# Kernel tuning notes

Hardware: AMD Instinct MI355X
Metric: run time of the kernel (lower is better)

Reference implementation:

```python
import jax, jax.numpy as jnp
import numpy as np

DIM = 512
HEADS = 8
DIM_HEAD = 64
ROT_DIM = DIM_HEAD // 2  # RotaryEmbedding(dim_head // 2)
B = 4
N = 8192


def rotate_every_two(x):
    # '... (d j) -> ... d j', j=2 ; (x1, x2) -> (-x2, x1) interleaved back
    x1 = x[..., 0::2]
    x2 = x[..., 1::2]
    return jnp.stack((-x2, x1), axis=-1).reshape(x.shape)


def apply_rotary_emb(freqs, t):
    # freqs: [1,1,n,rot_dim]; rotary on first rot_dim channels, passthrough rest
    rot_dim = freqs.shape[-1]
    t_rot, t_pass = t[..., :rot_dim], t[..., rot_dim:]
    t_rot = t_rot * jnp.cos(freqs) + rotate_every_two(t_rot) * jnp.sin(freqs)
    return jnp.concatenate((t_rot, t_pass), axis=-1)


def rotary_freqs(n):
    # lucidrains RotaryEmbedding(ROT_DIM): inv_freq over ROT_DIM//2, repeated r=2
    inv_freq = 1.0 / (10000.0 ** (jnp.arange(0, ROT_DIM, 2, dtype=jnp.float32) / ROT_DIM))
    f = jnp.arange(n, dtype=jnp.float32)[:, None] * inv_freq[None, :]  # [n, ROT_DIM//2]
    return jnp.repeat(f, 2, axis=-1)  # [n, ROT_DIM]


def setup_inputs() -> dict:
    key = jax.random.key(0)
    ks = jax.random.split(key, 8)
    inner = HEADS * DIM_HEAD
    s = lambda fan_in: 1.0 / np.sqrt(fan_in)
    return {
        "x": jax.random.normal(ks[0], (B, N, DIM), dtype=jnp.float32),
        "w_qkv": jax.random.uniform(ks[1], (DIM, inner * 3), jnp.float32, -s(DIM), s(DIM)),
        "w_q_logits": jax.random.uniform(ks[2], (DIM_HEAD, 1), jnp.float32, -s(DIM_HEAD), s(DIM_HEAD)),
        "w_k_logits": jax.random.uniform(ks[3], (DIM_HEAD // 2, 1), jnp.float32, -s(DIM_HEAD // 2), s(DIM_HEAD // 2)),
        "w_r": jax.random.uniform(ks[4], (DIM_HEAD // 2, DIM_HEAD), jnp.float32, -s(DIM_HEAD // 2), s(DIM_HEAD // 2)),
        "b_r": jax.random.uniform(ks[5], (DIM_HEAD,), jnp.float32, -s(DIM_HEAD // 2), s(DIM_HEAD // 2)),
        "w_out": jax.random.uniform(ks[6], (inner, DIM), jnp.float32, -s(inner), s(inner)),
        "b_out": jax.random.uniform(ks[7], (DIM,), jnp.float32, -s(inner), s(inner)),
    }


def reference(x, w_qkv, w_q_logits, w_k_logits, w_r, b_r, w_out, b_out):
    b, n, _ = x.shape
    h, d = HEADS, DIM_HEAD
    scale = d ** -0.5

    qkv = x @ w_qkv  # [b,n,3*h*d]
    q, k, v = jnp.split(qkv, 3, axis=-1)
    to_bhnd = lambda t: t.reshape(b, n, h, d).transpose(0, 2, 1, 3)
    q, k, v = to_bhnd(q), to_bhnd(k), to_bhnd(v)

    freqs = rotary_freqs(n)[None, None]  # [1,1,n,ROT_DIM]
    q_aggr = apply_rotary_emb(freqs, q)
    k_aggr = apply_rotary_emb(freqs, k)
    v_aggr = v

    q_attn = jax.nn.softmax((q @ w_q_logits)[..., 0] * scale, axis=-1)  # [b,h,n]
    global_q = jnp.einsum('bhn,bhnd->bhd', q_attn, q_aggr)[:, :, None]  # [b,h,1,d]

    kk = (k * global_q).reshape(b, h, n, d // 2, 2).sum(-1)  # sum adjacent pairs -> [b,h,n,d/2]
    k_attn = jax.nn.softmax((kk @ w_k_logits)[..., 0] * scale, axis=-1)
    global_k = jnp.einsum('bhn,bhnd->bhd', k_attn, k_aggr)[:, :, None]  # [b,h,1,d]

    u = (v_aggr * global_k).reshape(b, h, n, d // 2, 2).sum(-1)  # [b,h,n,d/2]
    r = u @ w_r + b_r  # [b,h,n,d]
    r = r + q
    r = r.transpose(0, 2, 1, 3).reshape(b, n, h * d)
    return r @ w_out + b_out
```

## Files before the change

kernel.cpp:

```cpp
#include <hip/hip_runtime.h>
#include <hip/hip_bf16.h>

typedef __attribute__((ext_vector_type(8))) short s16x8;
typedef __attribute__((ext_vector_type(4))) short s16x4;
typedef __attribute__((ext_vector_type(4))) float f32x4;

#define SEQ 8192

__device__ __forceinline__ float bf2f(short s){
  union { unsigned u; float f; } c; c.u = ((unsigned)(unsigned short)s) << 16; return c.f;
}
__device__ __forceinline__ short f2bf(float f){
  __hip_bfloat16 h = __float2bfloat16(f);
  short s; __builtin_memcpy(&s, &h, 2); return s;
}

__global__ __launch_bounds__(256) void build_tab64(float* __restrict__ ct, float* __restrict__ st){
  int idx = blockIdx.x*256 + threadIdx.x;
  int n = idx >> 6, d = idx & 63;
  float c, s;
  if (d < 32){
    float ex = -(float)(d & ~1) / 32.0f;
    float invf = __expf(ex * 9.210340371976184f);
    float f = (float)n * invf;
    c = cosf(f);
    s = sinf(f);
    s = (d & 1) ? s : -s;
  } else { c = 1.f; s = 0.f; }
  ct[idx] = c; st[idx] = s;
}

__global__ __launch_bounds__(256) void cvt_x(const float* __restrict__ in, __hip_bfloat16* __restrict__ out){
  int i = blockIdx.x*256 + threadIdx.x;
  float4 v = reinterpret_cast<const float4*>(in)[i];
  s16x4 o = { f2bf(v.x), f2bf(v.y), f2bf(v.z), f2bf(v.w) };
  reinterpret_cast<s16x4*>(out)[i] = o;
}

__global__ __launch_bounds__(256) void transpose_cvt(const float* __restrict__ in, __hip_bfloat16* __restrict__ out,
                                                     int R, int C){
  __shared__ float tile[32][33];
  int c0 = blockIdx.x*32, r0 = blockIdx.y*32;
  int tx = threadIdx.x & 31, ty = threadIdx.x >> 5;
  #pragma unroll
  for (int i = ty; i < 32; i += 8) tile[i][tx] = in[(size_t)(r0+i)*C + c0 + tx];
  __syncthreads();
  #pragma unroll
  for (int i = ty; i < 32; i += 8) out[(size_t)(c0+i)*R + r0 + tx] = __float2bfloat16(tile[tx][i]);
}

template<int MODE>
__global__ __launch_bounds__(512, 2) void gemm256(
    const __hip_bfloat16* __restrict__ A, const __hip_bfloat16* __restrict__ BT,
    int M, int Nn, int K,
    __hip_bfloat16* __restrict__ oQ, __hip_bfloat16* __restrict__ oK, __hip_bfloat16* __restrict__ oV,
    float* __restrict__ oF, const float* __restrict__ bias)
{
  __shared__ __align__(16) char lds[131072];
  const int t = threadIdx.x;
  const int lane = t & 63, wid = t >> 6;
  const int lr = lane & 15, lg = lane >> 4;
  const int wm128 = (wid >> 2) * 128;
  const int wn64  = (wid & 3) * 64;

  int nwg = gridDim.x, per = nwg >> 3, wg = blockIdx.x;
  int swz = (wg & 7) * per + (wg >> 3);
  int nblk = Nn >> 8;
  int bm = (swz / nblk) << 8;
  int bn = (swz % nblk) << 8;

  const int NKT = K >> 5;

  const __hip_bfloat16* spp[4];
  int dofs[4];
  #pragma unroll
  for (int i = 0; i < 4; ++i){
    int g = t + (i & 1)*512;
    int row = g >> 2, ch = g & 3;
    int sch = ch ^ ((row & 3) ^ ((row >> 2) & 3));
    spp[i] = (i < 2 ? A + (size_t)(bm + row)*K : BT + (size_t)(bn + row)*K) + sch*8;
    dofs[i] = ((i < 2) ? 0 : 16384) + g*16;
  }
  #define STG(i, kt) __builtin_amdgcn_global_load_lds( \
      (const __attribute__((address_space(1))) void*)(spp[i] + (size_t)(kt)*32), \
      (__attribute__((address_space(3))) void*)(lds + (((kt) & 3) << 15) + dofs[i]), 16, 0, 0)

  #pragma unroll
  for (int tl = 0; tl < 3; ++tl){ STG(0, tl); STG(1, tl); STG(2, tl); STG(3, tl); }

  f32x4 acc[8][4] = {};
  #define SWB(r) ((((r) & 3) ^ (((r) >> 2) & 3)) << 4)

  for (int kt = 0; kt < NKT; ++kt){
    if (kt + 2 < NKT)       asm volatile("s_waitcnt vmcnt(8)" ::: "memory");
    else if (kt + 2 == NKT) asm volatile("s_waitcnt vmcnt(4)" ::: "memory");
    else                    asm volatile("s_waitcnt vmcnt(0)" ::: "memory");
    __builtin_amdgcn_s_barrier();
    __builtin_amdgcn_sched_barrier(0);
    const char* lb = lds + ((kt & 3) << 15);
    s16x8 af[8], bfr[4];
    #pragma unroll
    for (int mi = 0; mi < 8; ++mi){
      int r = wm128 + mi*16 + lr;
      af[mi] = *reinterpret_cast<const s16x8*>(lb + r*64 + ((lg << 4) ^ SWB(r)));
    }
    #pragma unroll
    for (int ni = 0; ni < 4; ++ni){
      int r = wn64 + ni*16 + lr;
      bfr[ni] = *reinterpret_cast<const s16x8*>(lb + 16384 + r*64 + ((lg << 4) ^ SWB(r)));
    }
    if (kt + 3 < NKT){ STG(0, kt+3); STG(1, kt+3); STG(2, kt+3); STG(3, kt+3); }
    __builtin_amdgcn_s_setprio(1);
    #pragma unroll
    for (int mi = 0; mi < 8; ++mi)
      #pragma unroll
      for (int ni = 0; ni < 4; ++ni){
        if (MODE == 0) acc[mi][ni] = __builtin_amdgcn_mfma_f32_16x16x32_bf16(bfr[ni], af[mi], acc[mi][ni], 0, 0, 0);
        else           acc[mi][ni] = __builtin_amdgcn_mfma_f32_16x16x32_bf16(af[mi], bfr[ni], acc[mi][ni], 0, 0, 0);
      }
    __builtin_amdgcn_s_setprio(0);
  }
  __builtin_amdgcn_s_barrier();

  if (MODE == 0){
    char* reg = lds + wid*16384;
    #pragma unroll
    for (int mi = 0; mi < 8; ++mi){
      #pragma unroll
      for (int ni = 0; ni < 4; ++ni){
        int tok = mi*16 + lr;
        int cb = (ni*16 + lg*4) * 2;
        ushort4 w4;
        w4.x = (unsigned short)f2bf(acc[mi][ni][0]);
        w4.y = (unsigned short)f2bf(acc[mi][ni][1]);
        w4.z = (unsigned short)f2bf(acc[mi][ni][2]);
        w4.w = (unsigned short)f2bf(acc[mi][ni][3]);
        *reinterpret_cast<unsigned long long*>(reg + tok*128 + (cb ^ ((tok & 7) << 3))) =
            *reinterpret_cast<unsigned long long*>(&w4);
      }
    }
    int gcol = bn + wn64;
    int ts = gcol >> 9, rem = gcol & 511, h = rem >> 6;
    __hip_bfloat16* dstT = (ts == 0) ? oQ : ((ts == 1) ? oK : oV);
    int tokbase = bm + wm128;
    int bb = tokbase >> 13;
    dstT += ((size_t)(bb*8 + h)) << 19;
    #pragma unroll
    for (int p2 = 0; p2 < 16; ++p2){
      int tok = p2*8 + (lane >> 3);
      int b0 = (lane & 7) * 16;
      int sw = (tok & 7) << 3;
      unsigned long long u0 = *reinterpret_cast<const unsigned long long*>(reg + tok*128 + (b0 ^ sw));
      unsigned long long u1 = *reinterpret_cast<const unsigned long long*>(reg + tok*128 + ((b0 + 8) ^ sw));
      int n = (tokbase + tok) & 8191;
      unsigned long long o2[2] = { u0, u1 };
      *reinterpret_cast<s16x8*>(dstT + ((size_t)n << 6) + (lane & 7)*8) =
          *reinterpret_cast<const s16x8*>(o2);
    }
  } else {
    #pragma unroll
    for (int mi = 0; mi < 8; ++mi){
      #pragma unroll
      for (int ni = 0; ni < 4; ++ni){
        int gc = bn + wn64 + ni*16 + lr;
        float bv = bias[gc];
        #pragma unroll
        for (int j = 0; j < 4; ++j){
          int gr = bm + wm128 + mi*16 + lg*4 + j;
          oF[(size_t)gr*Nn + gc] = acc[mi][ni][j] + bv;
        }
      }
    }
  }
  #undef STG
  #undef SWB
}

__global__ __launch_bounds__(256) void fused_stats(
    const __hip_bfloat16* __restrict__ T, const float* __restrict__ svec, int svstride, float scale,
    const float* __restrict__ ct, const float* __restrict__ st, float* __restrict__ outp)
{
  int chunk = blockIdx.x, bh = blockIdx.y;
  int t = threadIdx.x, lane = t & 63, w = t >> 6;
  __shared__ float sv[64];
  __shared__ float ev[256];
  __shared__ float redv[4][64];
  __shared__ float rede[4];
  if (t < 64) sv[t] = svec[svstride*bh + t] * scale;
  __syncthreads();

  int n = chunk*256 + t;
  const __hip_bfloat16* row = T + ((size_t)bh*SEQ + n)*64;
  float s = 0.f;
  #pragma unroll
  for (int dv = 0; dv < 8; ++dv){
    s16x8 v8 = *reinterpret_cast<const s16x8*>(row + dv*8);
    #pragma unroll
    for (int e = 0; e < 8; ++e) s += bf2f(v8[e]) * sv[dv*8 + e];
  }
  ev[t] = __expf(s);
  __syncthreads();

  const short* Tsh = reinterpret_cast<const short*>(T + ((size_t)bh*SEQ)*64);
  float acc = 0.f, se = 0.f;
  int nb = chunk*256 + w*64;
  #pragma unroll 4
  for (int i = 0; i < 64; ++i){
    int n2 = nb + i;
    float e = ev[w*64 + i];
    float xv = bf2f(Tsh[(size_t)n2*64 + lane]);
    float xo = __shfl_xor(xv, 1, 64);
    acc += e * (xv*ct[n2*64 + lane] + xo*st[n2*64 + lane]);
    se += e;
  }
  redv[w][lane] = acc;
  if (lane == 0) rede[w] = se;
  __syncthreads();
  if (t < 64){
    float* ob = outp + (size_t)(bh*32 + chunk)*66;
    ob[2 + t] = redv[0][t] + redv[1][t] + redv[2][t] + redv[3][t];
    if (t == 0) ob[1] = rede[0] + rede[1] + rede[2] + rede[3];
  }
}

__global__ void final_combine(const float* __restrict__ parts, float* __restrict__ gvec,
                              const float* __restrict__ wkl, float* __restrict__ gqwk)
{
  int bh = blockIdx.x, d = threadIdx.x;
  const float* pp = parts + (size_t)bh*32*66;
  float tot = 0.f, g = 0.f;
  #pragma unroll 4
  for (int i = 0; i < 32; ++i){ tot += pp[i*66 + 1]; g += pp[i*66 + 2 + d]; }
  g /= tot;
  gvec[bh*64 + d] = g;
  if (gqwk) gqwk[bh*64 + d] = g * wkl[d >> 1] * 0.125f;
}

__global__ __launch_bounds__(256) void epilogue_r(
    const __hip_bfloat16* __restrict__ vT, const __hip_bfloat16* __restrict__ qT,
    const float* __restrict__ gk, const float* __restrict__ wr, const float* __restrict__ br,
    __hip_bfloat16* __restrict__ rb)
{
  int idx = blockIdx.x*256 + threadIdx.x;
  int bh = idx >> 13, nl = idx & 8191;
  int b = bh >> 3, h = bh & 7;
  const __hip_bfloat16* vrow = vT + (size_t)idx*64;
  const __hip_bfloat16* qrow = qT + (size_t)idx*64;
  const float* gkb = gk + bh*64;
  float u[32];
  #pragma unroll
  for (int dv = 0; dv < 8; ++dv){
    s16x8 v8 = *reinterpret_cast<const s16x8*>(vrow + dv*8);
    #pragma unroll
    for (int e = 0; e < 8; e += 2){
      int d = dv*8 + e;
      u[d >> 1] = bf2f(v8[e])*gkb[d] + bf2f(v8[e+1])*gkb[d+1];
    }
  }
  __hip_bfloat16* rrow = rb + ((size_t)(b*SEQ + nl))*512 + h*64;
  #pragma unroll 2
  for (int dv = 0; dv < 8; ++dv){
    s16x8 q8 = *reinterpret_cast<const s16x8*>(qrow + dv*8);
    s16x8 o8;
    #pragma unroll
    for (int e = 0; e < 8; ++e){
      int d = dv*8 + e;
      float a2 = br[d] + bf2f(q8[e]);
      #pragma unroll
      for (int j = 0; j < 32; ++j) a2 += u[j] * wr[j*64 + d];
      o8[e] = f2bf(a2);
    }
    *reinterpret_cast<s16x8*>(rrow + dv*8) = o8;
  }
}

extern "C" void kernel_launch(void* const* d_in, const int* in_sizes, int n_in,
                              void* d_out, int out_size, void* d_ws, size_t ws_size,
                              hipStream_t stream)
{
  (void)in_sizes; (void)n_in; (void)out_size; (void)ws_size;
  const float* x    = (const float*)d_in[0];
  const float* wqkv = (const float*)d_in[1];
  const float* wql  = (const float*)d_in[2];
  const float* wkl  = (const float*)d_in[3];
  const float* wr   = (const float*)d_in[4];
  const float* br   = (const float*)d_in[5];
  const float* wout = (const float*)d_in[6];
  const float* bout = (const float*)d_in[7];
  float* out = (float*)d_out;

  char* p = (char*)d_ws;
  auto alloc = [&](size_t bytes){ char* r = p; p += (bytes + 255) & ~(size_t)255; return r; };
  __hip_bfloat16* xb    = (__hip_bfloat16*)alloc(33554432);
  __hip_bfloat16* wqkvT = (__hip_bfloat16*)alloc(1572864);
  __hip_bfloat16* woutT = (__hip_bfloat16*)alloc(524288);
  __hip_bfloat16* qT = (__hip_bfloat16*)alloc(33554432);
  __hip_bfloat16* kT = (__hip_bfloat16*)alloc(33554432);
  __hip_bfloat16* vT = (__hip_bfloat16*)alloc(33554432);
  __hip_bfloat16* rb = (__hip_bfloat16*)alloc(33554432);
  float* ct     = (float*)alloc(2097152);
  float* st     = (float*)alloc(2097152);
  float* gq     = (float*)alloc(8192);
  float* gqwk   = (float*)alloc(8192);
  float* gk     = (float*)alloc(8192);

  float* partsQ = (float*)xb;
  float* partsK = partsQ + 32*32*66;

  build_tab64<<<2048, 256, 0, stream>>>(ct, st);
  cvt_x<<<16384, 256, 0, stream>>>(x, xb);
  transpose_cvt<<<dim3(48,16), 256, 0, stream>>>(wqkv, wqkvT, 512, 1536);
  transpose_cvt<<<dim3(16,16), 256, 0, stream>>>(wout, woutT, 512, 512);

  gemm256<0><<<768, 512, 0, stream>>>(xb, wqkvT, 32768, 1536, 512,
                                      qT, kT, vT, nullptr, nullptr);

  fused_stats<<<dim3(32,32), 256, 0, stream>>>(qT, wql, 0, 0.125f, ct, st, partsQ);
  final_combine<<<32, 64, 0, stream>>>(partsQ, gq, wkl, gqwk);
  fused_stats<<<dim3(32,32), 256, 0, stream>>>(kT, gqwk, 64, 1.0f, ct, st, partsK);
  final_combine<<<32, 64, 0, stream>>>(partsK, gk, nullptr, nullptr);

  epilogue_r<<<1024, 256, 0, stream>>>(vT, qT, gk, wr, br, rb);

  gemm256<1><<<256, 512, 0, stream>>>(rb, woutT, 32768, 512, 512,
                                      nullptr, nullptr, nullptr, out, bout);
}
```

Before: 211.0 us.

## Restructure GEMM main loop, shrink output tile, pack rotary table to bf16

The GEMM main loop now splits each K-step into two halves with interleaved LDS reads, staged global loads and barriers, so fewer A fragments are live at once. The output GEMM switches to 256x128 tiles with three LDS buffers and twice as many workgroups, and writes bias-added results as float4 stores. The rotary cos/sin tables are packed into one bf16x2 word per element to halve the table traffic in the stats kernels, and the QKV epilogue uses a different LDS swizzle. The extra barriers add synchronisation, and the bf16 rotary table reduces precision.

Result: slower. 218.6 us (+3.6%).

```diff
diff --git a/kernel.cpp b/kernel.cpp
--- a/kernel.cpp
+++ b/kernel.cpp
@@ -15,7 +15,7 @@
   short s; __builtin_memcpy(&s, &h, 2); return s;
 }
 
-__global__ __launch_bounds__(256) void build_tab64(float* __restrict__ ct, float* __restrict__ st){
+__global__ __launch_bounds__(256) void build_tab_pk(unsigned* __restrict__ tab){
   int idx = blockIdx.x*256 + threadIdx.x;
   int n = idx >> 6, d = idx & 63;
   float c, s;
@@ -27,7 +27,9 @@
     s = sinf(f);
     s = (d & 1) ? s : -s;
   } else { c = 1.f; s = 0.f; }
-  ct[idx] = c; st[idx] = s;
+  unsigned lo = (unsigned)(unsigned short)f2bf(c);
+  unsigned hi = (unsigned)(unsigned short)f2bf(s);
+  tab[idx] = lo | (hi << 16);
 }
 
 __global__ __launch_bounds__(256) void cvt_x(const float* __restrict__ in, __hip_bfloat16* __restrict__ out){
@@ -48,6 +50,9 @@
   #pragma unroll
   for (int i = ty; i < 32; i += 8) out[(size_t)(c0+i)*R + r0 + tx] = __float2bfloat16(tile[tx][i]);
 }
+
+#define SCHED0() __builtin_amdgcn_sched_barrier(0)
+#define BAR()    __builtin_amdgcn_s_barrier()
 
 template<int MODE>
 __global__ __launch_bounds__(512, 2) void gemm256(
@@ -56,71 +61,92 @@
     __hip_bfloat16* __restrict__ oQ, __hip_bfloat16* __restrict__ oK, __hip_bfloat16* __restrict__ oV,
     float* __restrict__ oF, const float* __restrict__ bias)
 {
-  __shared__ __align__(16) char lds[131072];
+  constexpr int NBUF  = (MODE == 0) ? 4 : 3;
+  constexpr int AHEAD = (MODE == 0) ? 3 : 2;
+  constexpr int BUFSZ = (MODE == 0) ? 32768 : 24576;
+  constexpr int NSTG  = (MODE == 0) ? 4 : 3;
+  constexpr int BN    = (MODE == 0) ? 256 : 128;
+  constexpr int MI    = (MODE == 0) ? 8 : 4;
+  __shared__ __align__(16) char lds[NBUF * BUFSZ];
+
   const int t = threadIdx.x;
   const int lane = t & 63, wid = t >> 6;
   const int lr = lane & 15, lg = lane >> 4;
-  const int wm128 = (wid >> 2) * 128;
-  const int wn64  = (wid & 3) * 64;
+  const int wm   = (MODE == 0) ? (wid >> 2) * 128 : (wid >> 1) * 64;
+  const int wn64 = (MODE == 0) ? (wid & 3) * 64   : (wid & 1) * 64;
 
   int nwg = gridDim.x, per = nwg >> 3, wg = blockIdx.x;
   int swz = (wg & 7) * per + (wg >> 3);
-  int nblk = Nn >> 8;
+  int nblk = Nn / BN;
   int bm = (swz / nblk) << 8;
-  int bn = (swz % nblk) << 8;
+  int bn = (swz % nblk) * BN;
 
   const int NKT = K >> 5;
 
-  const __hip_bfloat16* spp[4];
-  int dofs[4];
-  #pragma unroll
-  for (int i = 0; i < 4; ++i){
-    int g = t + (i & 1)*512;
+  const __hip_bfloat16* spp[NSTG];
+  int dofs[NSTG];
+  #pragma unroll
+  for (int i = 0; i < NSTG; ++i){
+    int g = (i < 2) ? (t + i*512) : ((MODE == 0) ? (t + (i-2)*512) : t);
     int row = g >> 2, ch = g & 3;
     int sch = ch ^ ((row & 3) ^ ((row >> 2) & 3));
     spp[i] = (i < 2 ? A + (size_t)(bm + row)*K : BT + (size_t)(bn + row)*K) + sch*8;
     dofs[i] = ((i < 2) ? 0 : 16384) + g*16;
   }
-  #define STG(i, kt) __builtin_amdgcn_global_load_lds( \
+  #define STG(i, kt, bufbase) __builtin_amdgcn_global_load_lds( \
       (const __attribute__((address_space(1))) void*)(spp[i] + (size_t)(kt)*32), \
-      (__attribute__((address_space(3))) void*)(lds + (((kt) & 3) << 15) + dofs[i]), 16, 0, 0)
-
-  #pragma unroll
-  for (int tl = 0; tl < 3; ++tl){ STG(0, tl); STG(1, tl); STG(2, tl); STG(3, tl); }
-
-  f32x4 acc[8][4] = {};
+      (__attribute__((address_space(3))) void*)(lds + (bufbase) + dofs[i]), 16, 0, 0)
+
+  #pragma unroll
+  for (int tl = 0; tl < AHEAD; ++tl)
+    #pragma unroll
+    for (int i = 0; i < NSTG; ++i) STG(i, tl, tl*BUFSZ);
+
+  f32x4 acc[MI][4] = {};
   #define SWB(r) ((((r) & 3) ^ (((r) >> 2) & 3)) << 4)
-
+  #define RD_A(h) _Pragma("unroll") for (int f = 0; f < 4; ++f){ \
+      int r = wm + (h)*64 + f*16 + lr; \
+      af[f] = *reinterpret_cast<const s16x8*>(lb + (r << 6) + ((lg << 4) ^ SWB(r))); }
+  #define RD_B() _Pragma("unroll") for (int f = 0; f < 4; ++f){ \
+      int r = wn64 + f*16 + lr; \
+      bfr[f] = *reinterpret_cast<const s16x8*>(lb + 16384 + (r << 6) + ((lg << 4) ^ SWB(r))); }
+  #define MFMA16(h) do { __builtin_amdgcn_s_setprio(1); \
+    _Pragma("unroll") for (int m2 = 0; m2 < 4; ++m2) \
+    _Pragma("unroll") for (int ni = 0; ni < 4; ++ni) \
+      acc[(h)*4+m2][ni] = __builtin_amdgcn_mfma_f32_16x16x32_bf16(bfr[ni], af[m2], acc[(h)*4+m2][ni], 0, 0, 0); \
+    __builtin_amdgcn_s_setprio(0); } while(0)
+
+  int rIdx = 0, sIdx = AHEAD % NBUF;
   for (int kt = 0; kt < NKT; ++kt){
-    if (kt + 2 < NKT)       asm volatile("s_waitcnt vmcnt(8)" ::: "memory");
-    else if (kt + 2 == NKT) asm volatile("s_waitcnt vmcnt(4)" ::: "memory");
-    else                    asm volatile("s_waitcnt vmcnt(0)" ::: "memory");
-    __builtin_amdgcn_s_barrier();
-    __builtin_amdgcn_sched_barrier(0);
-    const char* lb = lds + ((kt & 3) << 15);
-    s16x8 af[8], bfr[4];
-    #pragma unroll
-    for (int mi = 0; mi < 8; ++mi){
-      int r = wm128 + mi*16 + lr;
-      af[mi] = *reinterpret_cast<const s16x8*>(lb + r*64 + ((lg << 4) ^ SWB(r)));
-    }
-    #pragma unroll
-    for (int ni = 0; ni < 4; ++ni){
-      int r = wn64 + ni*16 + lr;
-      bfr[ni] = *reinterpret_cast<const s16x8*>(lb + 16384 + r*64 + ((lg << 4) ^ SWB(r)));
-    }
-    if (kt + 3 < NKT){ STG(0, kt+3); STG(1, kt+3); STG(2, kt+3); STG(3, kt+3); }
-    __builtin_amdgcn_s_setprio(1);
-    #pragma unroll
-    for (int mi = 0; mi < 8; ++mi)
-      #pragma unroll
-      for (int ni = 0; ni < 4; ++ni){
-        if (MODE == 0) acc[mi][ni] = __builtin_amdgcn_mfma_f32_16x16x32_bf16(bfr[ni], af[mi], acc[mi][ni], 0, 0, 0);
-        else           acc[mi][ni] = __builtin_amdgcn_mfma_f32_16x16x32_bf16(af[mi], bfr[ni], acc[mi][ni], 0, 0, 0);
-      }
-    __builtin_amdgcn_s_setprio(0);
-  }
-  __builtin_amdgcn_s_barrier();
+    if (MODE == 0){
+      if (kt + 2 < NKT)       asm volatile("s_waitcnt vmcnt(8)" ::: "memory");
+      else if (kt + 2 == NKT) asm volatile("s_waitcnt vmcnt(4)" ::: "memory");
+      else                    asm volatile("s_waitcnt vmcnt(0)" ::: "memory");
+    } else {
+      if (kt + 1 < NKT)       asm volatile("s_waitcnt vmcnt(3)" ::: "memory");
+      else                    asm volatile("s_waitcnt vmcnt(0)" ::: "memory");
+    }
+    SCHED0(); BAR(); SCHED0();
+    const char* lb = lds + rIdx*BUFSZ;
+    const int sb = sIdx*BUFSZ;
+    const bool stg = (kt + AHEAD) < NKT;
+    s16x8 af[4], bfr[4];
+    RD_A(0); RD_B();
+    if (stg){ STG(0, kt+AHEAD, sb); STG(1, kt+AHEAD, sb); }
+    if (MODE == 1 && stg){ STG(2, kt+AHEAD, sb); }
+    BAR(); SCHED0();
+    MFMA16(0);
+    if (MODE == 0){
+      BAR(); SCHED0();
+      RD_A(1);
+      if (stg){ STG(2, kt+AHEAD, sb); STG(3, kt+AHEAD, sb); }
+      BAR(); SCHED0();
+      MFMA16(1);
+    }
+    rIdx = (rIdx + 1 == NBUF) ? 0 : rIdx + 1;
+    sIdx = (sIdx + 1 == NBUF) ? 0 : sIdx + 1;
+  }
+  BAR();
 
   if (MODE == 0){
     char* reg = lds + wid*16384;
@@ -129,29 +155,30 @@
       #pragma unroll
       for (int ni = 0; ni < 4; ++ni){
         int tok = mi*16 + lr;
-        int cb = (ni*16 + lg*4) * 2;
+        int sl = (ni*4 + lg) ^ (tok & 15);
         ushort4 w4;
         w4.x = (unsigned short)f2bf(acc[mi][ni][0]);
         w4.y = (unsigned short)f2bf(acc[mi][ni][1]);
         w4.z = (unsigned short)f2bf(acc[mi][ni][2]);
         w4.w = (unsigned short)f2bf(acc[mi][ni][3]);
-        *reinterpret_cast<unsigned long long*>(reg + tok*128 + (cb ^ ((tok & 7) << 3))) =
+        *reinterpret_cast<unsigned long long*>(reg + tok*128 + sl*8) =
             *reinterpret_cast<unsigned long long*>(&w4);
       }
     }
+    asm volatile("s_waitcnt lgkmcnt(0)" ::: "memory");
+    SCHED0();
     int gcol = bn + wn64;
     int ts = gcol >> 9, rem = gcol & 511, h = rem >> 6;
     __hip_bfloat16* dstT = (ts == 0) ? oQ : ((ts == 1) ? oK : oV);
-    int tokbase = bm + wm128;
+    int tokbase = bm + wm;
     int bb = tokbase >> 13;
     dstT += ((size_t)(bb*8 + h)) << 19;
     #pragma unroll
     for (int p2 = 0; p2 < 16; ++p2){
       int tok = p2*8 + (lane >> 3);
-      int b0 = (lane & 7) * 16;
-      int sw = (tok & 7) << 3;
-      unsigned long long u0 = *reinterpret_cast<const unsigned long long*>(reg + tok*128 + (b0 ^ sw));
-      unsigned long long u1 = *reinterpret_cast<const unsigned long long*>(reg + tok*128 + ((b0 + 8) ^ sw));
+      int l0 = (lane & 7) * 2;
+      unsigned long long u0 = *reinterpret_cast<const unsigned long long*>(reg + tok*128 + ((l0 ^ (tok & 15)))*8);
+      unsigned long long u1 = *reinterpret_cast<const unsigned long long*>(reg + tok*128 + (((l0+1) ^ (tok & 15)))*8);
       int n = (tokbase + tok) & 8191;
       unsigned long long o2[2] = { u0, u1 };
       *reinterpret_cast<s16x8*>(dstT + ((size_t)n << 6) + (lane & 7)*8) =
@@ -159,26 +186,31 @@
     }
   } else {
     #pragma unroll
-    for (int mi = 0; mi < 8; ++mi){
+    for (int mi = 0; mi < MI; ++mi){
       #pragma unroll
       for (int ni = 0; ni < 4; ++ni){
-        int gc = bn + wn64 + ni*16 + lr;
-        float bv = bias[gc];
-        #pragma unroll
-        for (int j = 0; j < 4; ++j){
-          int gr = bm + wm128 + mi*16 + lg*4 + j;
-          oF[(size_t)gr*Nn + gc] = acc[mi][ni][j] + bv;
-        }
+        int gc = bn + wn64 + ni*16 + lg*4;
+        int gr = bm + wm + mi*16 + lr;
+        float4 bv = *reinterpret_cast<const float4*>(bias + gc);
+        float4 o;
+        o.x = acc[mi][ni][0] + bv.x;
+        o.y = acc[mi][ni][1] + bv.y;
+        o.z = acc[mi][ni][2] + bv.z;
+        o.w = acc[mi][ni][3] + bv.w;
+        *reinterpret_cast<float4*>(oF + (size_t)gr*Nn + gc) = o;
       }
     }
   }
   #undef STG
   #undef SWB
+  #undef RD_A
+  #undef RD_B
+  #undef MFMA16
 }
 
 __global__ __launch_bounds__(256) void fused_stats(
     const __hip_bfloat16* __restrict__ T, const float* __restrict__ svec, int svstride, float scale,
-    const float* __restrict__ ct, const float* __restrict__ st, float* __restrict__ outp)
+    const unsigned* __restrict__ tab, float* __restrict__ outp)
 {
   int chunk = blockIdx.x, bh = blockIdx.y;
   int t = threadIdx.x, lane = t & 63, w = t >> 6;
@@ -210,7 +242,10 @@
     float e = ev[w*64 + i];
     float xv = bf2f(Tsh[(size_t)n2*64 + lane]);
     float xo = __shfl_xor(xv, 1, 64);
-    acc += e * (xv*ct[n2*64 + lane] + xo*st[n2*64 + lane]);
+    unsigned cs = tab[n2*64 + lane];
+    float c  = bf2f((short)(cs & 0xffff));
+    float s2 = bf2f((short)(cs >> 16));
+    acc += e * (xv*c + xo*s2);
     se += e;
   }
   redv[w][lane] = acc;
@@ -298,8 +333,7 @@
   __hip_bfloat16* kT = (__hip_bfloat16*)alloc(33554432);
   __hip_bfloat16* vT = (__hip_bfloat16*)alloc(33554432);
   __hip_bfloat16* rb = (__hip_bfloat16*)alloc(33554432);
-  float* ct     = (float*)alloc(2097152);
-  float* st     = (float*)alloc(2097152);
+  unsigned* tab = (unsigned*)alloc(2097152);
   float* gq     = (float*)alloc(8192);
   float* gqwk   = (float*)alloc(8192);
   float* gk     = (float*)alloc(8192);
@@ -307,7 +341,7 @@
   float* partsQ = (float*)xb;
   float* partsK = partsQ + 32*32*66;
 
-  build_tab64<<<2048, 256, 0, stream>>>(ct, st);
+  build_tab_pk<<<2048, 256, 0, stream>>>(tab);
   cvt_x<<<16384, 256, 0, stream>>>(x, xb);
   transpose_cvt<<<dim3(48,16), 256, 0, stream>>>(wqkv, wqkvT, 512, 1536);
   transpose_cvt<<<dim3(16,16), 256, 0, stream>>>(wout, woutT, 512, 512);
@@ -315,13 +349,13 @@
   gemm256<0><<<768, 512, 0, stream>>>(xb, wqkvT, 32768, 1536, 512,
                                       qT, kT, vT, nullptr, nullptr);
 
-  fused_stats<<<dim3(32,32), 256, 0, stream>>>(qT, wql, 0, 0.125f, ct, st, partsQ);
+  fused_stats<<<dim3(32,32), 256, 0, stream>>>(qT, wql, 0, 0.125f, tab, partsQ);
   final_combine<<<32, 64, 0, stream>>>(partsQ, gq, wkl, gqwk);
-  fused_stats<<<dim3(32,32), 256, 0, stream>>>(kT, gqwk, 64, 1.0f, ct, st, partsK);
+  fused_stats<<<dim3(32,32), 256, 0, stream>>>(kT, gqwk, 64, 1.0f, tab, partsK);
   final_combine<<<32, 64, 0, stream>>>(partsK, gk, nullptr, nullptr);
 
   epilogue_r<<<1024, 256, 0, stream>>>(vT, qT, gk, wr, br, rb);
 
-  gemm256<1><<<256, 512, 0, stream>>>(rb, woutT, 32768, 512, 512,
+  gemm256<1><<<512, 512, 0, stream>>>(rb, woutT, 32768, 512, 512,
                                       nullptr, nullptr, nullptr, out, bout);
 }
```
